# Kernel tuning notes

Measured on AMD Instinct MI355X. Metric: run time of the kernel, lower is better.

Reference implementation:

```python
import jax, jax.numpy as jnp
import numpy as np

N = 4096      # tokens per modality
DIM = 514     # input feature dim
OUT = 256     # out_dim (per-head width, head=1)
NC = 2        # num_classes
LN_EPS = 1e-5


def setup_inputs() -> dict:
    key = jax.random.key(0)
    ks = jax.random.split(key, 12)
    def nrm(k, shape, s=0.02):
        return jax.random.normal(k, shape, dtype=jnp.float32) * s
    return {
        "t1": jax.random.normal(ks[0], (N, DIM), dtype=jnp.float32),
        "t2": jax.random.normal(ks[1], (N, DIM), dtype=jnp.float32),
        "t1c": jax.random.normal(ks[2], (N, DIM), dtype=jnp.float32),
        "Wqkv1": nrm(ks[3], (DIM, 3 * OUT)), "bqkv1": jnp.zeros((3 * OUT,), jnp.float32),
        "Wqkv2": nrm(ks[4], (DIM, 3 * OUT)), "bqkv2": jnp.zeros((3 * OUT,), jnp.float32),
        "Wqkv3": nrm(ks[5], (DIM, 3 * OUT)), "bqkv3": jnp.zeros((3 * OUT,), jnp.float32),
        "Wo1": nrm(ks[6], (2 * OUT, DIM)), "bo1": jnp.zeros((DIM,), jnp.float32),
        "Wo2": nrm(ks[7], (2 * OUT, DIM)), "bo2": jnp.zeros((DIM,), jnp.float32),
        "Wo3": nrm(ks[8], (2 * OUT, DIM)), "bo3": jnp.zeros((DIM,), jnp.float32),
        "ln_g": jnp.ones((3 * DIM,), jnp.float32),
        "ln_b": jnp.zeros((3 * DIM,), jnp.float32),
        "Wh": nrm(ks[9], (3 * DIM, NC)), "bh": jnp.zeros((NC,), jnp.float32),
    }


def _forward(t1, t2, t1c, Wqkv1, bqkv1, Wqkv2, bqkv2, Wqkv3, bqkv3,
             Wo1, bo1, Wo2, bo2, Wo3, bo3, ln_g, ln_b, Wh, bh):
    # QKV projections (head=1 so no head reshape needed)
    q1, k1, v1 = jnp.split(t1 @ Wqkv1 + bqkv1, 3, axis=-1)   # each [n, OUT]
    q2, k2, v2 = jnp.split(t2 @ Wqkv2 + bqkv2, 3, axis=-1)
    q3, k3, v3 = jnp.split(t1c @ Wqkv3 + bqkv3, 3, axis=-1)

    # Six cross-attention instances batched into one group dim g=6.
    # Order: out12, out13, out21, out23, out31, out32  (q_x attends to k_y/v_y)
    qs = jnp.stack([q2, q3, q1, q3, q1, q2])                  # [6, n, OUT]
    ks_ = jnp.stack([k1, k1, k2, k2, k3, k3])
    vs = jnp.stack([v1, v1, v2, v2, v3, v3])
    # NOTE: original code applies NO 1/sqrt(d) scale
    attn = jax.nn.softmax(jnp.einsum('gid,gjd->gij', qs, ks_), axis=-1)
    outs = jnp.einsum('gij,gjd->gid', attn, vs)               # [6, n, OUT]
    out12, out13, out21, out23, out31, out32 = outs

    # residual add with duplicated keys, then per-modality output proj + residual
    t1r = jnp.concatenate([out21, out31], -1) + jnp.concatenate([k1, k1], -1)
    t2r = jnp.concatenate([out12, out32], -1) + jnp.concatenate([k2, k2], -1)
    t3r = jnp.concatenate([out13, out23], -1) + jnp.concatenate([k3, k3], -1)
    a1 = t1r @ Wo1 + bo1 + t1                                 # [n, DIM]
    a2 = t2r @ Wo2 + bo2 + t2
    a3 = t3r @ Wo3 + bo3 + t1c

    atten = jnp.concatenate([a1, a2, a3], -1)                 # [n, 3*DIM]
    mu = jnp.mean(atten, axis=-1, keepdims=True)
    var = jnp.var(atten, axis=-1, keepdims=True)
    normed = (atten - mu) * jax.lax.rsqrt(var + LN_EPS) * ln_g + ln_b
    out = normed @ Wh + bh                                    # [n, NC]
    feat = atten[None]                                        # [1, n, 3*DIM]
    return out, feat


def reference(t1, t2, t1c, Wqkv1, bqkv1, Wqkv2, bqkv2, Wqkv3, bqkv3,
              Wo1, bo1, Wo2, bo2, Wo3, bo3, ln_g, ln_b, Wh, bh):
    return _forward(t1, t2, t1c, Wqkv1, bqkv1, Wqkv2, bqkv2, Wqkv3, bqkv3,
                    Wo1, bo1, Wo2, bo2, Wo3, bo3, ln_g, ln_b, Wh, bh)
```

## Files before the change

kernel.cpp:

```cpp
#include <hip/hip_runtime.h>
#include <hip/hip_bf16.h>

typedef unsigned short u16;
typedef unsigned int u32;
typedef __attribute__((ext_vector_type(8))) __bf16 bf16x8;
typedef __attribute__((ext_vector_type(16))) float f32x16;

#define N_TOK 4096
#define DIMF  514
#define KPAD  544
#define OUT3  768
#define OUTD  256
#define RDIM  512
#define FDIM  1542
#define LOG2E 1.4426950408889634f
#define SHIFT2 23.083120654223415f
#define NCHUNK 4
#define KTILES ((N_TOK / NCHUNK) / 32)

__device__ __forceinline__ bf16x8 ld_frag(const u16* p) {
    return __builtin_bit_cast(bf16x8, *reinterpret_cast<const uint4*>(p));
}
__device__ __forceinline__ u16 f2bf(float x) {
    return __builtin_bit_cast(u16, __float2bfloat16(x));
}
__device__ __forceinline__ float bf2f(u16 u) {
    return __bfloat162float(__builtin_bit_cast(__hip_bfloat16, u));
}
__device__ __forceinline__ f32x16 mfma_b(bf16x8 a, bf16x8 b, f32x16 c) {
    return __builtin_amdgcn_mfma_f32_32x32x16_bf16(a, b, c, 0, 0, 0);
}
__device__ __forceinline__ void gl_lds16(const u16* g, u16* l) {
    __builtin_amdgcn_global_load_lds(
        (const __attribute__((address_space(1))) void*)(g),
        (__attribute__((address_space(3))) void*)(l), 16, 0, 0);
}

__global__ __launch_bounds__(256, 1) void prep_tA(
    const float* __restrict__ t1, const float* __restrict__ t2,
    const float* __restrict__ t1c, u16* __restrict__ tA)
{
    int idx = blockIdx.x * 256 + threadIdx.x;
    int m = idx / (N_TOK * KPAD);
    int rem = idx - m * (N_TOK * KPAD);
    int row = rem / KPAD;
    int col = rem - row * KPAD;
    const float* t = (m == 0) ? t1 : (m == 1) ? t2 : t1c;
    tA[idx] = (col < DIMF) ? f2bf(t[row * DIMF + col]) : (u16)0;
}

__global__ __launch_bounds__(256, 1) void transpose_w(
    const float* __restrict__ Wa, const float* __restrict__ Wb,
    const float* __restrict__ Wc, u16* __restrict__ Out,
    int R, int C, int OS)
{
    const int bx = blockIdx.x;
    const int by = blockIdx.y;
    const int m  = blockIdx.z;
    const float* W = (m == 0) ? Wa : (m == 1) ? Wb : Wc;
    u16* O = Out + (size_t)m * C * OS;

    __shared__ u16 Lt[64 * 72];
    const int tid = threadIdx.x;
    const int c0 = bx * 64, r0 = by * 64;
#pragma unroll
    for (int it = 0; it < 16; it++) {
        int i = it * 256 + tid;
        int ri = i >> 6, ci = i & 63;
        int rr = r0 + ri, cc = c0 + ci;
        float v = (rr < R && cc < C) ? W[rr * C + cc] : 0.f;
        Lt[ci * 72 + ri] = f2bf(v);
    }
    __syncthreads();
#pragma unroll
    for (int it = 0; it < 2; it++) {
        int i = it * 256 + tid;
        int ci = i >> 3, seg = i & 7;
        int n = c0 + ci, col = r0 + seg * 8;
        if (n < C && col < OS)
            *reinterpret_cast<uint4*>(&O[(size_t)n * OS + col]) =
                *reinterpret_cast<const uint4*>(&Lt[ci * 72 + seg * 8]);
    }
}

__global__ __launch_bounds__(256, 1) void qkv_gemm(
    const u16* __restrict__ tA, const u16* __restrict__ WqkvT,
    const float* __restrict__ b1, const float* __restrict__ b2, const float* __restrict__ b3,
    u16* __restrict__ qbuf, u16* __restrict__ kbuf, u16* __restrict__ vT)
{
    const int mt = blockIdx.x, nt = blockIdx.y, mod = blockIdx.z;
    const u16* A = tA + mod * (N_TOK * KPAD);
    const u16* B = WqkvT + mod * (OUT3 * KPAD);
    const float* bias = (mod == 0) ? b1 : (mod == 1) ? b2 : b3;

    __shared__ alignas(16) u16 smem[128 * 136];
    u16* Al = smem;
    u16* Bl = smem + 128 * 40;

    const int tid = threadIdx.x;
    const int lane = tid & 63;
    const int w = tid >> 6;
    const int wm = w & 1, wn = w >> 1;
    const int l31 = lane & 31, h = lane >> 5;

    f32x16 acc[2][2];
#pragma unroll
    for (int i = 0; i < 2; i++)
#pragma unroll
        for (int j = 0; j < 2; j++)
#pragma unroll
            for (int r = 0; r < 16; r++) acc[i][j][r] = 0.f;

    for (int kt = 0; kt < KPAD / 32; kt++) {
#pragma unroll
        for (int it = 0; it < 2; it++) {
            int idx = it * 256 + tid;
            int row = idx >> 2;
            int c8 = (idx & 3) * 8;
            uint4 va = *reinterpret_cast<const uint4*>(&A[(mt * 128 + row) * KPAD + kt * 32 + c8]);
            *reinterpret_cast<uint4*>(&Al[row * 40 + c8]) = va;
            uint4 vb = *reinterpret_cast<const uint4*>(&B[(nt * 128 + row) * KPAD + kt * 32 + c8]);
            *reinterpret_cast<uint4*>(&Bl[row * 40 + c8]) = vb;
        }
        __syncthreads();
#pragma unroll
        for (int kc = 0; kc < 2; kc++) {
            bf16x8 af[2], bfr[2];
#pragma unroll
            for (int mr = 0; mr < 2; mr++)
                af[mr] = ld_frag(&Al[(wm * 64 + mr * 32 + l31) * 40 + kc * 16 + h * 8]);
#pragma unroll
            for (int nr = 0; nr < 2; nr++)
                bfr[nr] = ld_frag(&Bl[(wn * 64 + nr * 32 + l31) * 40 + kc * 16 + h * 8]);
#pragma unroll
            for (int mr = 0; mr < 2; mr++)
#pragma unroll
                for (int nr = 0; nr < 2; nr++)
                    acc[mr][nr] = mfma_b(af[mr], bfr[nr], acc[mr][nr]);
        }
        __syncthreads();
    }

    if (nt < 4) {
        u16* qb = qbuf + mod * (N_TOK * OUTD);
        u16* kb = kbuf + mod * (N_TOK * OUTD);
#pragma unroll
        for (int mr = 0; mr < 2; mr++)
#pragma unroll
            for (int nr = 0; nr < 2; nr++)
#pragma unroll
                for (int r = 0; r < 16; r++) {
                    int row = mt * 128 + wm * 64 + mr * 32 + (r & 3) + 8 * (r >> 2) + 4 * h;
                    int col = nt * 128 + wn * 64 + nr * 32 + l31;
                    float sc = (col < 256) ? LOG2E : 1.0f;
                    u16 bv = f2bf((acc[mr][nr][r] + bias[col]) * sc);
                    if (col < 256) qb[row * OUTD + col] = bv;
                    else           kb[row * OUTD + (col - 256)] = bv;
                }
    } else {
        u16* Tv = smem;
#pragma unroll
        for (int mr = 0; mr < 2; mr++)
#pragma unroll
            for (int nr = 0; nr < 2; nr++)
#pragma unroll
                for (int r = 0; r < 16; r++) {
                    int row_l = wm * 64 + mr * 32 + (r & 3) + 8 * (r >> 2) + 4 * h;
                    int d_l = wn * 64 + nr * 32 + l31;
                    int col_g = nt * 128 + d_l;
                    Tv[d_l * 136 + row_l] = f2bf(acc[mr][nr][r] + bias[col_g]);
                }
        __syncthreads();
        u16* vb = vT + mod * (OUTD * N_TOK);
        const int colbase = (nt - 4) * 128;
#pragma unroll
        for (int it = 0; it < 8; it++) {
            int i = it * 256 + tid;
            int cc = i >> 4, seg = i & 15;
            *reinterpret_cast<uint4*>(&vb[(colbase + cc) * N_TOK + mt * 128 + seg * 8]) =
                *reinterpret_cast<const uint4*>(&Tv[cc * 136 + seg * 8]);
        }
    }
}

__global__ __launch_bounds__(256, 2) void attn_kernel(
    const u16* __restrict__ qbuf, const u16* __restrict__ kbuf,
    const u16* __restrict__ vT, u16* __restrict__ Opart, float* __restrict__ lpart)
{
    const int qt = blockIdx.x;
    const int g  = blockIdx.y;
    const int c  = blockIdx.z;
    const int kv = g >> 1;
    const int mn = (kv == 0) ? 1 : 0;
    const int mx = (kv == 2) ? 1 : 2;
    const int qm = (g & 1) ? mx : mn;

    const u16* Qg = qbuf + qm * (N_TOK * OUTD);
    const u16* Kg = kbuf + kv * (N_TOK * OUTD);
    const u16* Vg = vT + kv * (OUTD * N_TOK);
    u16* Op = Opart + ((size_t)(c * 6 + g) * N_TOK + qt * 128) * OUTD;
    float* lp = lpart + (c * 6 + g) * N_TOK + qt * 128;

    __shared__ alignas(16) u16 Fbuf[2][32 * 512];

    const int tid = threadIdx.x;
    const int lane = tid & 63;
    const int w = tid >> 6;
    const int l31 = lane & 31, h = lane >> 5;
    const int q0 = qt * 128 + w * 32;

    auto stage = [&](int k0, u16* dst) {
        if (w < 2) {
#pragma unroll
            for (int fi = 0; fi < 8; fi++) {
                int dc = w * 8 + fi;
                gl_lds16(&Kg[(k0 + l31) * OUTD + dc * 16 + h * 8], dst + dc * 512);
            }
        } else {
#pragma unroll
            for (int fi = 0; fi < 8; fi++) {
                int f = (w - 2) * 8 + fi;
                int nb = f >> 1, half = f & 1;
                gl_lds16(&Vg[(nb * 32 + l31) * N_TOK + k0 + half * 16 + h * 8],
                         dst + (16 + f) * 512);
            }
        }
    };

    const int k0base = c * (N_TOK / NCHUNK);

    stage(k0base, Fbuf[0]);

    bf16x8 qf[16];
#pragma unroll
    for (int dc = 0; dc < 16; dc++)
        qf[dc] = ld_frag(&Qg[(q0 + l31) * OUTD + dc * 16 + h * 8]);

    f32x16 Oacc[8];
#pragma unroll
    for (int nb = 0; nb < 8; nb++)
#pragma unroll
        for (int r = 0; r < 16; r++) Oacc[nb][r] = 0.f;
    float lsum = 0.f;

    __syncthreads();

    for (int kt = 0; kt < KTILES; kt++) {
        const int p = kt & 1;
        if (kt + 1 < KTILES) stage(k0base + (kt + 1) * 32, Fbuf[p ^ 1]);
        const u16* FB = Fbuf[p];

        f32x16 S;
#pragma unroll
        for (int r = 0; r < 16; r++) S[r] = 0.f;
#pragma unroll
        for (int dc = 0; dc < 16; dc++) {
            bf16x8 kf = ld_frag(&FB[dc * 512 + lane * 8]);
            S = mfma_b(kf, qf[dc], S);
        }

        float e[16];
#pragma unroll
        for (int r = 0; r < 16; r++) { e[r] = exp2f(S[r] - SHIFT2); lsum += e[r]; }
        u32 pk[8];
#pragma unroll
        for (int i = 0; i < 8; i++)
            pk[i] = (u32)f2bf(e[2 * i]) | ((u32)f2bf(e[2 * i + 1]) << 16);
        u32 x[8];
#pragma unroll
        for (int i = 0; i < 8; i++)
            x[i] = (u32)__shfl_xor((int)pk[i], 32, 64);
        uint4 b0, b1;
        b0.x = h ? x[2] : pk[0]; b0.y = h ? x[3] : pk[1];
        b0.z = h ? pk[2] : x[0]; b0.w = h ? pk[3] : x[1];
        b1.x = h ? x[6] : pk[4]; b1.y = h ? x[7] : pk[5];
        b1.z = h ? pk[6] : x[4]; b1.w = h ? pk[7] : x[5];
        bf16x8 pb0 = __builtin_bit_cast(bf16x8, b0);
        bf16x8 pb1 = __builtin_bit_cast(bf16x8, b1);

#pragma unroll
        for (int nb = 0; nb < 8; nb++) {
            bf16x8 vf0 = ld_frag(&FB[(16 + 2 * nb) * 512 + lane * 8]);
            bf16x8 vf1 = ld_frag(&FB[(17 + 2 * nb) * 512 + lane * 8]);
            Oacc[nb] = mfma_b(vf0, pb0, Oacc[nb]);
            Oacc[nb] = mfma_b(vf1, pb1, Oacc[nb]);
        }
        __syncthreads();
    }

    lsum += __shfl_xor(lsum, 32, 64);
    if (lane < 32) lp[w * 32 + lane] = lsum;

    float* Tb = reinterpret_cast<float*>(&Fbuf[0][0]) + w * (32 * 33);
#pragma unroll
    for (int nb = 0; nb < 8; nb++) {
#pragma unroll
        for (int r = 0; r < 16; r++)
            Tb[((r & 3) + 8 * (r >> 2) + 4 * h) * 33 + l31] = Oacc[nb][r];
        __builtin_amdgcn_s_waitcnt(0);
#pragma unroll
        for (int qq = 0; qq < 16; qq++) {
            float v = Tb[l31 * 33 + qq * 2 + h];
            Op[(w * 32 + qq * 2 + h) * OUTD + nb * 32 + l31] = f2bf(v);
        }
        __builtin_amdgcn_s_waitcnt(0);
    }
}

__global__ __launch_bounds__(256, 1) void combine_kernel(
    const u16* __restrict__ Opart, const float* __restrict__ lpart,
    const u16* __restrict__ kbuf, u16* __restrict__ rbuf)
{
    const int q = blockIdx.x;
    const int g = blockIdx.y;
    const int d = threadIdx.x;
    const int kv = g >> 1;
    const int mn = (kv == 0) ? 1 : 0;
    const int mx = (kv == 2) ? 1 : 2;
    const int qm = (g & 1) ? mx : mn;
    const int sm = (qm == 0) ? 1 : 0;
    const int slot = (kv == sm) ? 0 : 1;

    float o = 0.f, l = 0.f;
#pragma unroll
    for (int c = 0; c < NCHUNK; c++) {
        o += bf2f(Opart[((size_t)(c * 6 + g) * N_TOK + q) * OUTD + d]);
        l += lpart[(c * 6 + g) * N_TOK + q];
    }
    float res = o / l + bf2f(kbuf[qm * (N_TOK * OUTD) + q * OUTD + d]);
    rbuf[qm * (size_t)(N_TOK * RDIM) + q * RDIM + slot * OUTD + d] = f2bf(res);
}

__global__ __launch_bounds__(256, 1) void proj_gemm(
    const u16* __restrict__ rbuf, const u16* __restrict__ WoT,
    const float* __restrict__ bo1, const float* __restrict__ bo2, const float* __restrict__ bo3,
    const float* __restrict__ t1, const float* __restrict__ t2, const float* __restrict__ t1c,
    float* __restrict__ feat)
{
    const int mt = blockIdx.x, nt = blockIdx.y, mod = blockIdx.z;
    const u16* A = rbuf + mod * (N_TOK * RDIM);
    const u16* B = WoT + mod * (DIMF * RDIM);
    const float* bias = (mod == 0) ? bo1 : (mod == 1) ? bo2 : bo3;
    const float* tres = (mod == 0) ? t1 : (mod == 1) ? t2 : t1c;

    __shared__ alignas(16) u16 Al[128 * 40];
    __shared__ alignas(16) u16 Bl[128 * 40];

    const int tid = threadIdx.x;
    const int lane = tid & 63;
    const int w = tid >> 6;
    const int wm = w & 1, wn = w >> 1;
    const int l31 = lane & 31, h = lane >> 5;

    f32x16 acc[2][2];
#pragma unroll
    for (int i = 0; i < 2; i++)
#pragma unroll
        for (int j = 0; j < 2; j++)
#pragma unroll
            for (int r = 0; r < 16; r++) acc[i][j][r] = 0.f;

    for (int kt = 0; kt < RDIM / 32; kt++) {
#pragma unroll
        for (int it = 0; it < 2; it++) {
            int idx = it * 256 + tid;
            int row = idx >> 2;
            int c8 = (idx & 3) * 8;
            uint4 va = *reinterpret_cast<const uint4*>(&A[(mt * 128 + row) * RDIM + kt * 32 + c8]);
            *reinterpret_cast<uint4*>(&Al[row * 40 + c8]) = va;
            int n = nt * 128 + row;
            uint4 vb;
            if (n < DIMF) vb = *reinterpret_cast<const uint4*>(&B[n * RDIM + kt * 32 + c8]);
            else { vb.x = vb.y = vb.z = vb.w = 0u; }
            *reinterpret_cast<uint4*>(&Bl[row * 40 + c8]) = vb;
        }
        __syncthreads();
#pragma unroll
        for (int kc = 0; kc < 2; kc++) {
            bf16x8 af[2], bfr[2];
#pragma unroll
            for (int mr = 0; mr < 2; mr++)
                af[mr] = ld_frag(&Al[(wm * 64 + mr * 32 + l31) * 40 + kc * 16 + h * 8]);
#pragma unroll
            for (int nr = 0; nr < 2; nr++)
                bfr[nr] = ld_frag(&Bl[(wn * 64 + nr * 32 + l31) * 40 + kc * 16 + h * 8]);
#pragma unroll
            for (int mr = 0; mr < 2; mr++)
#pragma unroll
                for (int nr = 0; nr < 2; nr++)
                    acc[mr][nr] = mfma_b(af[mr], bfr[nr], acc[mr][nr]);
        }
        __syncthreads();
    }

#pragma unroll
    for (int mr = 0; mr < 2; mr++)
#pragma unroll
        for (int nr = 0; nr < 2; nr++)
#pragma unroll
            for (int r = 0; r < 16; r++) {
                int row = mt * 128 + wm * 64 + mr * 32 + (r & 3) + 8 * (r >> 2) + 4 * h;
                int col = nt * 128 + wn * 64 + nr * 32 + l31;
                if (col < DIMF) {
                    float v = acc[mr][nr][r] + bias[col] + tres[row * DIMF + col];
                    feat[row * FDIM + mod * DIMF + col] = v;
                }
            }
}

__global__ __launch_bounds__(256, 1) void ln_head(
    const float* __restrict__ feat, const float* __restrict__ gam,
    const float* __restrict__ bet, const float* __restrict__ Wh,
    const float* __restrict__ bh, float* __restrict__ out)
{
    const int row = blockIdx.x;
    const float* x = feat + row * FDIM;
    const int tid = threadIdx.x;
    float v[7];
    float s = 0.f, ss = 0.f;
#pragma unroll
    for (int i = 0; i < 7; i++) {
        int idx = tid + i * 256;
        float val = (idx < FDIM) ? x[idx] : 0.f;
        v[i] = val; s += val; ss += val * val;
    }
#pragma unroll
    for (int m = 1; m < 64; m <<= 1) { s += __shfl_xor(s, m, 64); ss += __shfl_xor(ss, m, 64); }
    __shared__ float red[8];
    const int w = tid >> 6, lane = tid & 63;
    if (lane == 0) { red[w] = s; red[4 + w] = ss; }
    __syncthreads();
    s = red[0] + red[1] + red[2] + red[3];
    ss = red[4] + red[5] + red[6] + red[7];
    const float mu = s / (float)FDIM;
    const float var = ss / (float)FDIM - mu * mu;
    const float rstd = rsqrtf(var + 1e-5f);
    float a0 = 0.f, a1 = 0.f;
#pragma unroll
    for (int i = 0; i < 7; i++) {
        int idx = tid + i * 256;
        if (idx < FDIM) {
            float nv = (v[i] - mu) * rstd * gam[idx] + bet[idx];
            a0 += nv * Wh[idx * 2];
            a1 += nv * Wh[idx * 2 + 1];
        }
    }
#pragma unroll
    for (int m = 1; m < 64; m <<= 1) { a0 += __shfl_xor(a0, m, 64); a1 += __shfl_xor(a1, m, 64); }
    __shared__ float red2[8];
    if (lane == 0) { red2[w] = a0; red2[4 + w] = a1; }
    __syncthreads();
    if (tid == 0) {
        out[row * 2 + 0] = red2[0] + red2[1] + red2[2] + red2[3] + bh[0];
        out[row * 2 + 1] = red2[4] + red2[5] + red2[6] + red2[7] + bh[1];
    }
}

extern "C" void kernel_launch(void* const* d_in, const int* in_sizes, int n_in,
                              void* d_out, int out_size, void* d_ws, size_t ws_size,
                              hipStream_t stream)
{
    const float* t1    = (const float*)d_in[0];
    const float* t2    = (const float*)d_in[1];
    const float* t1c   = (const float*)d_in[2];
    const float* Wqkv1 = (const float*)d_in[3];
    const float* bqkv1 = (const float*)d_in[4];
    const float* Wqkv2 = (const float*)d_in[5];
    const float* bqkv2 = (const float*)d_in[6];
    const float* Wqkv3 = (const float*)d_in[7];
    const float* bqkv3 = (const float*)d_in[8];
    const float* Wo1   = (const float*)d_in[9];
    const float* bo1   = (const float*)d_in[10];
    const float* Wo2   = (const float*)d_in[11];
    const float* bo2   = (const float*)d_in[12];
    const float* Wo3   = (const float*)d_in[13];
    const float* bo3   = (const float*)d_in[14];
    const float* ln_g  = (const float*)d_in[15];
    const float* ln_b  = (const float*)d_in[16];
    const float* Wh    = (const float*)d_in[17];
    const float* bh    = (const float*)d_in[18];

    char* ws = (char*)d_ws;
    size_t off = 0;
    u16* tA    = (u16*)(ws + off); off += (size_t)3 * N_TOK * KPAD * 2;
    u16* WqkvT = (u16*)(ws + off); off += (size_t)3 * OUT3 * KPAD * 2;
    u16* WoT   = (u16*)(ws + off); off += (size_t)3 * DIMF * RDIM * 2;
    u16* qbuf  = (u16*)(ws + off); off += (size_t)3 * N_TOK * OUTD * 2;
    u16* kbuf  = (u16*)(ws + off); off += (size_t)3 * N_TOK * OUTD * 2;
    u16* vT    = (u16*)(ws + off); off += (size_t)3 * OUTD * N_TOK * 2;
    u16* rbuf  = (u16*)(ws + off); off += (size_t)3 * N_TOK * RDIM * 2;
    u16* Opart = (u16*)(ws + off); off += (size_t)NCHUNK * 6 * N_TOK * OUTD * 2;
    float* lpart = (float*)(ws + off); off += (size_t)NCHUNK * 6 * N_TOK * 4;

    float* out  = (float*)d_out;
    float* feat = out + N_TOK * 2;

    prep_tA<<<(3 * N_TOK * KPAD) / 256, 256, 0, stream>>>(t1, t2, t1c, tA);

    transpose_w<<<dim3(12, 9, 3), 256, 0, stream>>>(
        Wqkv1, Wqkv2, Wqkv3, WqkvT, DIMF, OUT3, KPAD);
    transpose_w<<<dim3(9, 8, 3), 256, 0, stream>>>(
        Wo1, Wo2, Wo3, WoT, RDIM, DIMF, RDIM);

    qkv_gemm<<<dim3(32, 6, 3), 256, 0, stream>>>(
        tA, WqkvT, bqkv1, bqkv2, bqkv3, qbuf, kbuf, vT);

    attn_kernel<<<dim3(32, 6, NCHUNK), 256, 0, stream>>>(qbuf, kbuf, vT, Opart, lpart);

    combine_kernel<<<dim3(N_TOK, 6), 256, 0, stream>>>(Opart, lpart, kbuf, rbuf);

    proj_gemm<<<dim3(32, 5, 3), 256, 0, stream>>>(
        rbuf, WoT, bo1, bo2, bo3, t1, t2, t1c, feat);

    ln_head<<<4096, 256, 0, stream>>>(feat, ln_g, ln_b, Wh, bh, out);
}
```

Baseline: 348.0 us.

## Process 64 query rows per wave in attention to reuse K/V fragments

The attention kernel drops from 4 to 2 waves per block, and each wave now handles two 32-row query sub-tiles. Every K and V fragment read from LDS feeds two MFMAs instead of one, halving LDS read traffic per unit of compute. The cost is roughly double the accumulator and Q-fragment registers per wave (launch bounds 128,1), which lowers occupancy and may cause spills. Each wave also now stages twice as many global-to-LDS loads.

```diff
diff --git a/kernel.cpp b/kernel.cpp
--- a/kernel.cpp
+++ b/kernel.cpp
@@ -183,7 +183,7 @@
     }
 }
 
-__global__ __launch_bounds__(256, 2) void attn_kernel(
+__global__ __launch_bounds__(128, 1) void attn_kernel(
     const u16* __restrict__ qbuf, const u16* __restrict__ kbuf,
     const u16* __restrict__ vT, u16* __restrict__ Opart, float* __restrict__ lpart)
 {
@@ -207,19 +207,16 @@
     const int lane = tid & 63;
     const int w = tid >> 6;
     const int l31 = lane & 31, h = lane >> 5;
-    const int q0 = qt * 128 + w * 32;
+    const int q0 = qt * 128 + w * 64;
 
     auto stage = [&](int k0, u16* dst) {
-        if (w < 2) {
-#pragma unroll
-            for (int fi = 0; fi < 8; fi++) {
-                int dc = w * 8 + fi;
+        if (w == 0) {
+#pragma unroll
+            for (int dc = 0; dc < 16; dc++)
                 gl_lds16(&Kg[(k0 + l31) * OUTD + dc * 16 + h * 8], dst + dc * 512);
-            }
         } else {
 #pragma unroll
-            for (int fi = 0; fi < 8; fi++) {
-                int f = (w - 2) * 8 + fi;
+            for (int f = 0; f < 16; f++) {
                 int nb = f >> 1, half = f & 1;
                 gl_lds16(&Vg[(nb * 32 + l31) * N_TOK + k0 + half * 16 + h * 8],
                          dst + (16 + f) * 512);
@@ -231,17 +228,21 @@
 
     stage(k0base, Fbuf[0]);
 
-    bf16x8 qf[16];
-#pragma unroll
-    for (int dc = 0; dc < 16; dc++)
-        qf[dc] = ld_frag(&Qg[(q0 + l31) * OUTD + dc * 16 + h * 8]);
-
-    f32x16 Oacc[8];
-#pragma unroll
-    for (int nb = 0; nb < 8; nb++)
-#pragma unroll
-        for (int r = 0; r < 16; r++) Oacc[nb][r] = 0.f;
-    float lsum = 0.f;
+    bf16x8 qf[2][16];
+#pragma unroll
+    for (int half = 0; half < 2; half++)
+#pragma unroll
+        for (int dc = 0; dc < 16; dc++)
+            qf[half][dc] = ld_frag(&Qg[(q0 + half * 32 + l31) * OUTD + dc * 16 + h * 8]);
+
+    f32x16 Oacc[2][8];
+#pragma unroll
+    for (int half = 0; half < 2; half++)
+#pragma unroll
+        for (int nb = 0; nb < 8; nb++)
+#pragma unroll
+            for (int r = 0; r < 16; r++) Oacc[half][nb][r] = 0.f;
+    float lsum0 = 0.f, lsum1 = 0.f;
 
     __syncthreads();
 
@@ -250,61 +251,75 @@
         if (kt + 1 < KTILES) stage(k0base + (kt + 1) * 32, Fbuf[p ^ 1]);
         const u16* FB = Fbuf[p];
 
-        f32x16 S;
-#pragma unroll
-        for (int r = 0; r < 16; r++) S[r] = 0.f;
+        f32x16 S0, S1;
+#pragma unroll
+        for (int r = 0; r < 16; r++) { S0[r] = 0.f; S1[r] = 0.f; }
 #pragma unroll
         for (int dc = 0; dc < 16; dc++) {
             bf16x8 kf = ld_frag(&FB[dc * 512 + lane * 8]);
-            S = mfma_b(kf, qf[dc], S);
-        }
-
-        float e[16];
-#pragma unroll
-        for (int r = 0; r < 16; r++) { e[r] = exp2f(S[r] - SHIFT2); lsum += e[r]; }
-        u32 pk[8];
-#pragma unroll
-        for (int i = 0; i < 8; i++)
-            pk[i] = (u32)f2bf(e[2 * i]) | ((u32)f2bf(e[2 * i + 1]) << 16);
-        u32 x[8];
-#pragma unroll
-        for (int i = 0; i < 8; i++)
-            x[i] = (u32)__shfl_xor((int)pk[i], 32, 64);
-        uint4 b0, b1;
-        b0.x = h ? x[2] : pk[0]; b0.y = h ? x[3] : pk[1];
-        b0.z = h ? pk[2] : x[0]; b0.w = h ? pk[3] : x[1];
-        b1.x = h ? x[6] : pk[4]; b1.y = h ? x[7] : pk[5];
-        b1.z = h ? pk[6] : x[4]; b1.w = h ? pk[7] : x[5];
-        bf16x8 pb0 = __builtin_bit_cast(bf16x8, b0);
-        bf16x8 pb1 = __builtin_bit_cast(bf16x8, b1);
+            S0 = mfma_b(kf, qf[0][dc], S0);
+            S1 = mfma_b(kf, qf[1][dc], S1);
+        }
+
+        bf16x8 pb0a, pb0b, pb1a, pb1b;
+        auto softmax = [&](const f32x16& S, float& lsum, bf16x8& pba, bf16x8& pbb) {
+            float e[16];
+#pragma unroll
+            for (int r = 0; r < 16; r++) { e[r] = exp2f(S[r] - SHIFT2); lsum += e[r]; }
+            u32 pk[8];
+#pragma unroll
+            for (int i = 0; i < 8; i++)
+                pk[i] = (u32)f2bf(e[2 * i]) | ((u32)f2bf(e[2 * i + 1]) << 16);
+            u32 x[8];
+#pragma unroll
+            for (int i = 0; i < 8; i++)
+                x[i] = (u32)__shfl_xor((int)pk[i], 32, 64);
+            uint4 b0, b1;
+            b0.x = h ? x[2] : pk[0]; b0.y = h ? x[3] : pk[1];
+            b0.z = h ? pk[2] : x[0]; b0.w = h ? pk[3] : x[1];
+            b1.x = h ? x[6] : pk[4]; b1.y = h ? x[7] : pk[5];
+            b1.z = h ? pk[6] : x[4]; b1.w = h ? pk[7] : x[5];
+            pba = __builtin_bit_cast(bf16x8, b0);
+            pbb = __builtin_bit_cast(bf16x8, b1);
+        };
+        softmax(S0, lsum0, pb0a, pb0b);
+        softmax(S1, lsum1, pb1a, pb1b);
 
 #pragma unroll
         for (int nb = 0; nb < 8; nb++) {
             bf16x8 vf0 = ld_frag(&FB[(16 + 2 * nb) * 512 + lane * 8]);
             bf16x8 vf1 = ld_frag(&FB[(17 + 2 * nb) * 512 + lane * 8]);
-            Oacc[nb] = mfma_b(vf0, pb0, Oacc[nb]);
-            Oacc[nb] = mfma_b(vf1, pb1, Oacc[nb]);
+            Oacc[0][nb] = mfma_b(vf0, pb0a, Oacc[0][nb]);
+            Oacc[0][nb] = mfma_b(vf1, pb0b, Oacc[0][nb]);
+            Oacc[1][nb] = mfma_b(vf0, pb1a, Oacc[1][nb]);
+            Oacc[1][nb] = mfma_b(vf1, pb1b, Oacc[1][nb]);
         }
         __syncthreads();
     }
 
-    lsum += __shfl_xor(lsum, 32, 64);
-    if (lane < 32) lp[w * 32 + lane] = lsum;
+    lsum0 += __shfl_xor(lsum0, 32, 64);
+    lsum1 += __shfl_xor(lsum1, 32, 64);
+    if (lane < 32) {
+        lp[w * 64 + lane] = lsum0;
+        lp[w * 64 + 32 + lane] = lsum1;
+    }
 
     float* Tb = reinterpret_cast<float*>(&Fbuf[0][0]) + w * (32 * 33);
 #pragma unroll
-    for (int nb = 0; nb < 8; nb++) {
-#pragma unroll
-        for (int r = 0; r < 16; r++)
-            Tb[((r & 3) + 8 * (r >> 2) + 4 * h) * 33 + l31] = Oacc[nb][r];
-        __builtin_amdgcn_s_waitcnt(0);
-#pragma unroll
-        for (int qq = 0; qq < 16; qq++) {
-            float v = Tb[l31 * 33 + qq * 2 + h];
-            Op[(w * 32 + qq * 2 + h) * OUTD + nb * 32 + l31] = f2bf(v);
-        }
-        __builtin_amdgcn_s_waitcnt(0);
-    }
+    for (int half = 0; half < 2; half++)
+#pragma unroll
+        for (int nb = 0; nb < 8; nb++) {
+#pragma unroll
+            for (int r = 0; r < 16; r++)
+                Tb[((r & 3) + 8 * (r >> 2) + 4 * h) * 33 + l31] = Oacc[half][nb][r];
+            __builtin_amdgcn_s_waitcnt(0);
+#pragma unroll
+            for (int qq = 0; qq < 16; qq++) {
+                float v = Tb[l31 * 33 + qq * 2 + h];
+                Op[(w * 64 + half * 32 + qq * 2 + h) * OUTD + nb * 32 + l31] = f2bf(v);
+            }
+            __builtin_amdgcn_s_waitcnt(0);
+        }
 }
 
 __global__ __launch_bounds__(256, 1) void combine_kernel(
@@ -505,7 +520,7 @@
     qkv_gemm<<<dim3(32, 6, 3), 256, 0, stream>>>(
         tA, WqkvT, bqkv1, bqkv2, bqkv3, qbuf, kbuf, vT);
 
-    attn_kernel<<<dim3(32, 6, NCHUNK), 256, 0, stream>>>(qbuf, kbuf, vT, Opart, lpart);
+    attn_kernel<<<dim3(32, 6, NCHUNK), 128, 0, stream>>>(qbuf, kbuf, vT, Opart, lpart);
 
     combine_kernel<<<dim3(N_TOK, 6), 256, 0, stream>>>(Opart, lpart, kbuf, rbuf);
 
```

After: 414.7 us. +19.1%, slower.
